# Kernel optimization log

Measured on AMD Instinct MI355X. Metric: run time of the kernel, lower is better.

## Reference

```python
import jax, jax.numpy as jnp
import numpy as np
from jax import lax

B, T, V, E, H, C, K = 256, 512, 50000, 128, 256, 128, 2


def setup_inputs() -> dict:
    key = jax.random.key(0)
    ks = jax.random.split(key, 16)
    s = lambda *sh: 1.0 / np.sqrt(sh[0])
    return {
        "input_current": jax.random.randint(ks[0], (B, T), 0, V, dtype=jnp.int32),
        "input_left": jax.random.randint(ks[1], (B, T), 0, V, dtype=jnp.int32),
        "input_right": jax.random.randint(ks[2], (B, T), 0, V, dtype=jnp.int32),
        "emb": jax.random.normal(ks[3], (V, E), jnp.float32) * 0.05,
        "Wf": jax.random.normal(ks[4], (E, H), jnp.float32) * s(E),
        "Uf": jax.random.normal(ks[5], (H, H), jnp.float32) * s(H),
        "bf": jnp.zeros((H,), jnp.float32),
        "Wb": jax.random.normal(ks[6], (E, H), jnp.float32) * s(E),
        "Ub": jax.random.normal(ks[7], (H, H), jnp.float32) * s(H),
        "bb": jnp.zeros((H,), jnp.float32),
        "Wc": jax.random.normal(ks[8], (2 * H + E, C), jnp.float32) * s(2 * H + E),
        "bc": jnp.zeros((C,), jnp.float32),
        "Wd": jax.random.normal(ks[9], (C, K), jnp.float32) * s(C),
        "bd": jnp.zeros((K,), jnp.float32),
    }


def _simple_rnn(x, W, U, b):
    # x: [B,T,E] -> outputs [B,T,H]; h_t = tanh(x_t W + b + h_{t-1} U)
    xw = jnp.einsum("bte,eh->bth", x, W) + b  # precompute input projection
    h0 = jnp.zeros((x.shape[0], U.shape[0]), x.dtype)

    def step(h, xw_t):
        h = jnp.tanh(xw_t + h @ U)
        return h, h

    _, hs = lax.scan(step, h0, jnp.swapaxes(xw, 0, 1))  # scan over time
    return jnp.swapaxes(hs, 0, 1)


def reference(input_current, input_left, input_right, emb, Wf, Uf, bf, Wb, Ub, bb, Wc, bc, Wd, bd):
    e_cur = emb[input_current]  # [B,T,E]
    e_left = emb[input_left]
    e_right = emb[input_right]
    x_left = _simple_rnn(e_left, Wf, Uf, bf)  # [B,T,H]
    # go_backwards RNN: process reversed sequence, then model reverses back
    x_right = _simple_rnn(e_right[:, ::-1], Wb, Ub, bb)[:, ::-1]  # [B,T,H]
    x = jnp.concatenate([x_left, e_cur, x_right], axis=2)  # [B,T,2H+E]
    x = jnp.tanh(jnp.einsum("btd,dc->btc", x, Wc) + bc)  # Conv1D k=1 + tanh
    x = jnp.max(x, axis=1)  # GlobalMaxPooling1D
    return jax.nn.sigmoid(x @ Wd + bd)  # [B,K]
```

## Files before the change

kernel.cpp:

```cpp
#include <hip/hip_runtime.h>
#include <hip/hip_bf16.h>


#define B_ 256
#define T_ 512
#define E_ 128
#define H_ 256
#define C_ 128

typedef __attribute__((ext_vector_type(8))) short short8;
typedef __attribute__((ext_vector_type(4))) float float4v;
typedef __attribute__((ext_vector_type(2))) unsigned int uint2v;

__device__ inline unsigned short f2bf(float f) {
  unsigned u = __float_as_uint(f);
  u += 0x7fffu + ((u >> 16) & 1u);
  return (unsigned short)(u >> 16);
}
__device__ inline unsigned pkbf(float a, float b) {
  __hip_bfloat162 h2 = __float22bfloat162_rn(float2{a, b});
  union { __hip_bfloat162 h; unsigned u; } cv;
  cv.h = h2;
  return cv.u;
}
__device__ inline float lo16f(unsigned u) { return __uint_as_float(u << 16); }
__device__ inline float hi16f(unsigned u) { return __uint_as_float(u & 0xffff0000u); }
__device__ inline float fast_tanh(float x) {
  float e = __expf(2.f * x);
  float r = __builtin_amdgcn_rcpf(e + 1.f);
  return __builtin_fmaf(-2.f, r, 1.f);
}
__device__ inline unsigned enc_f(float f) {
  unsigned u = __float_as_uint(f);
  return (u & 0x80000000u) ? ~u : (u | 0x80000000u);
}
__device__ inline float dec_f(unsigned key) {
  unsigned bits = (key & 0x80000000u) ? (key ^ 0x80000000u) : ~key;
  return __uint_as_float(bits);
}
__device__ inline void sync_lds() {
  asm volatile("s_waitcnt lgkmcnt(0)\n\ts_barrier" ::: "memory");
}

__device__ inline void st_agent(unsigned short* p, uint2v v) {
  union { uint2v v2; unsigned long long u; } cv;
  cv.v2 = v;
  __hip_atomic_store(reinterpret_cast<unsigned long long*>(p), cv.u,
                     __ATOMIC_RELAXED, __HIP_MEMORY_SCOPE_AGENT);
}

__device__ inline void wait_flag_ge(const int* f, int v) {
  if (__hip_atomic_load(f, __ATOMIC_RELAXED, __HIP_MEMORY_SCOPE_AGENT) < v) {
    while (__hip_atomic_load(f, __ATOMIC_RELAXED, __HIP_MEMORY_SCOPE_AGENT) <
           v)
      __builtin_amdgcn_s_sleep(8);
  }
  (void)__hip_atomic_load(f, __ATOMIC_ACQUIRE, __HIP_MEMORY_SCOPE_AGENT);
}

__global__ __launch_bounds__(256) void prep_kernel(
    const float* __restrict__ Wf, const float* __restrict__ Wb,
    const float* __restrict__ Wc, const float* __restrict__ Uf,
    const float* __restrict__ Ub,
    unsigned short* __restrict__ WfT, unsigned short* __restrict__ WbT,
    unsigned short* __restrict__ WcT, unsigned short* __restrict__ UfT,
    unsigned short* __restrict__ UbT, unsigned int* __restrict__ pooled,
    int* __restrict__ flags) {
  int gid = blockIdx.x * 256 + threadIdx.x;
  int stride = gridDim.x * 256;
  for (int i = gid; i < 128 * 256; i += stride) {
    int k = i >> 8, n = i & 255;
    WfT[n * 128 + k] = f2bf(Wf[i]);
    WbT[n * 128 + k] = f2bf(Wb[i]);
  }
  for (int i = gid; i < 640 * 128; i += stride) {
    int k = i >> 7, n = i & 127;
    WcT[n * 640 + k] = f2bf(Wc[i]);
  }
  for (int i = gid; i < 256 * 256; i += stride) {
    int k = i >> 8, n = i & 255;
    UfT[n * 256 + k] = f2bf(Uf[i]);
    UbT[n * 256 + k] = f2bf(Ub[i]);
  }
  for (int i = gid; i < B_ * C_; i += stride) pooled[i] = 0u;
  for (int i = gid; i < 1024; i += stride) flags[i] = 0;
}

__global__ __launch_bounds__(512, 1) void fused_kernel(
    const int* __restrict__ idxL, const int* __restrict__ idxR,
    const int* __restrict__ idxC, const float* __restrict__ emb,
    const unsigned short* __restrict__ WfT,
    const unsigned short* __restrict__ WbT,
    const float* __restrict__ bfv, const float* __restrict__ bbv,
    const unsigned short* __restrict__ UfT,
    const unsigned short* __restrict__ UbT,
    const unsigned short* __restrict__ WcT, const float* __restrict__ bc,
    unsigned short* x, unsigned int* __restrict__ pooled,
    int* __restrict__ flags) {
  const int blk = blockIdx.x;
  const int tid = threadIdx.x;
  const int lane = tid & 63, q = lane >> 4, l15 = lane & 15;

  __shared__ __attribute__((aligned(16))) unsigned short hbuf[2][16][280];

  if (blk < 32) {
    const int dir = blk & 1;
    const int btile = blk >> 1;
    const int b0 = btile * 16;
    const unsigned short* __restrict__ UT = dir ? UbT : UfT;
    const int xoff = dir ? 384 : 0;
    const int tstep = dir ? -1 : 1;
    const int t0 = dir ? (T_ - 1) : 0;
    const ptrdiff_t dstep = (ptrdiff_t)tstep * 640;
    const int wv8 = tid >> 6;
    int* fl = flags + (dir * 16 + btile) * 32;

    unsigned short* hb0 = &hbuf[0][0][0];
    unsigned short* hb1 = &hbuf[1][0][0];
    for (int i = tid; i < 2 * 16 * 280; i += 512) hb0[i] = 0;

    if (wv8 >= 4) {
      __syncthreads();
#pragma unroll 1
      for (int p = 0; p < 256; ++p) {
        sync_lds();
        sync_lds();
      }
      return;
    }
    const int wv = wv8;

    short8 ufr[4][8];
#pragma unroll
    for (int mt = 0; mt < 4; ++mt)
#pragma unroll
      for (int kt = 0; kt < 8; ++kt)
        ufr[mt][kt] = *(const short8*)(UT + (64 * wv + 16 * mt + l15) * H_ +
                                       kt * 32 + q * 8);

    int lastc = dir ? 31 : 0;
    wait_flag_ge(fl + lastc, 1);

    unsigned short* ptrS[4];
    const unsigned short* ptrL[4];
    uint2v curA[4], curB[4];
#pragma unroll
    for (int mt = 0; mt < 4; ++mt) {
      unsigned short* bt = x + (size_t)(b0 + 4 * wv + mt) * T_ * 640 + xoff +
                           lane * 4 + (ptrdiff_t)t0 * 640;
      curA[mt] = *(const uint2v*)(bt);
      curB[mt] = *(const uint2v*)(bt + dstep);
      ptrS[mt] = bt;
      ptrL[mt] = bt + 2 * dstep;
    }

    const unsigned lrd = l15 * 280;
    const unsigned lwr = l15 * 280 + 64 * wv;

    __syncthreads();

#pragma unroll 1
    for (int p = 0; p < 256; ++p) {
      int c = dir ? ((508 - 2 * p) >> 4) : ((2 * p + 3) >> 4);
      c = c < 0 ? 0 : (c > 31 ? 31 : c);
      if (c != lastc) {
        wait_flag_ge(fl + c, 1);
        lastc = c;
      }
      uint2v ldA[4], ldB[4];
      if (p < 255) {
#pragma unroll
        for (int mt = 0; mt < 4; ++mt) {
          ldA[mt] = *(const uint2v*)(ptrL[mt]);
          ldB[mt] = *(const uint2v*)(ptrL[mt] + dstep);
        }
      } else {
#pragma unroll
        for (int mt = 0; mt < 4; ++mt) {
          ldA[mt] = curA[mt];
          ldB[mt] = curB[mt];
        }
      }
#pragma unroll
      for (int mt = 0; mt < 4; ++mt) ptrL[mt] += 2 * dstep;

      {
        short8 afr[8];
#pragma unroll
        for (int kt = 0; kt < 8; ++kt)
          afr[kt] = *(const short8*)(hb0 + lrd + kt * 32 + q * 8);
        float4v acc[4];
#pragma unroll
        for (int mt = 0; mt < 4; ++mt)
          acc[mt] = (float4v){lo16f(curA[mt].x), hi16f(curA[mt].x),
                              lo16f(curA[mt].y), hi16f(curA[mt].y)};
#pragma unroll
        for (int kt = 0; kt < 8; ++kt)
#pragma unroll
          for (int mt = 0; mt < 4; ++mt)
            acc[mt] = __builtin_amdgcn_mfma_f32_16x16x32_bf16(
                ufr[mt][kt], afr[kt], acc[mt], 0, 0, 0);
#pragma unroll
        for (int mt = 0; mt < 4; ++mt) {
          uint2v hv = {pkbf(fast_tanh(acc[mt][0]), fast_tanh(acc[mt][1])),
                       pkbf(fast_tanh(acc[mt][2]), fast_tanh(acc[mt][3]))};
          *(uint2v*)(hb1 + lwr + 16 * mt + 4 * q) = hv;
          st_agent(ptrS[mt], hv);
        }
      }
      sync_lds();

      {
        short8 afr[8];
#pragma unroll
        for (int kt = 0; kt < 8; ++kt)
          afr[kt] = *(const short8*)(hb1 + lrd + kt * 32 + q * 8);
        float4v acc[4];
#pragma unroll
        for (int mt = 0; mt < 4; ++mt)
          acc[mt] = (float4v){lo16f(curB[mt].x), hi16f(curB[mt].x),
                              lo16f(curB[mt].y), hi16f(curB[mt].y)};
#pragma unroll
        for (int kt = 0; kt < 8; ++kt)
#pragma unroll
          for (int mt = 0; mt < 4; ++mt)
            acc[mt] = __builtin_amdgcn_mfma_f32_16x16x32_bf16(
                ufr[mt][kt], afr[kt], acc[mt], 0, 0, 0);
#pragma unroll
        for (int mt = 0; mt < 4; ++mt) {
          uint2v hv = {pkbf(fast_tanh(acc[mt][0]), fast_tanh(acc[mt][1])),
                       pkbf(fast_tanh(acc[mt][2]), fast_tanh(acc[mt][3]))};
          *(uint2v*)(hb0 + lwr + 16 * mt + 4 * q) = hv;
          st_agent(ptrS[mt] + dstep, hv);
        }
      }
#pragma unroll
      for (int mt = 0; mt < 4; ++mt) {
        ptrS[mt] += 2 * dstep;
        curA[mt] = ldA[mt];
        curB[mt] = ldB[mt];
      }
      if (((p + 1) & 7) == 0) {
        asm volatile("s_waitcnt vmcnt(0) lgkmcnt(0)\n\ts_barrier" ::: "memory");
        if (tid == 0) {
          const int cdone = dir ? (32 - ((p + 1) >> 3)) : (((p + 1) >> 3) - 1);
          __hip_atomic_store(fl + cdone, 2, __ATOMIC_RELAXED,
                             __HIP_MEMORY_SCOPE_AGENT);
        }
      } else {
        sync_lds();
      }
    }
    return;
  }

  if (blk < 1056) {
    const int b2 = blk - 32;
    const int z = b2 >> 5, r = b2 & 31;
    const int btile = r & 15, dirg = r >> 4;
    const int chunk = dirg ? (31 - z) : z;
    const int w8 = tid >> 6;
    const int g = w8 >> 2, wv = w8 & 3;
    const int t0 = chunk * 16 + g * 8;
    const int b0 = btile * 16;
    const int* __restrict__ idx = dirg ? idxR : idxL;
    const unsigned short* __restrict__ WT = dirg ? WbT : WfT;
    const float* __restrict__ bias = dirg ? bbv : bfv;

    short8 wfr[4][4];
#pragma unroll
    for (int mt = 0; mt < 4; ++mt)
#pragma unroll
      for (int kt = 0; kt < 4; ++kt)
        wfr[mt][kt] = *(const short8*)(WT + (64 * wv + 16 * mt + l15) * 128 +
                                       kt * 32 + q * 8);
    float4v bv[4];
#pragma unroll
    for (int mt = 0; mt < 4; ++mt)
      bv[mt] = *(const float4v*)(bias + 64 * wv + 16 * mt + 4 * q);

    int er[8];
#pragma unroll
    for (int j = 0; j < 8; ++j) er[j] = idx[(b0 + l15) * T_ + t0 + j];

    float4v g0[8];
#pragma unroll
    for (int kt = 0; kt < 4; ++kt) {
      const float* p8 = emb + (size_t)er[0] * E_ + kt * 32 + q * 8;
      g0[2 * kt] = *(const float4v*)p8;
      g0[2 * kt + 1] = *(const float4v*)(p8 + 4);
    }

#pragma unroll 1
    for (int j = 0; j < 8; ++j) {
      float4v gn[8];
      if (j < 7) {
#pragma unroll
        for (int kt = 0; kt < 4; ++kt) {
          const float* p8 = emb + (size_t)er[j + 1] * E_ + kt * 32 + q * 8;
          gn[2 * kt] = *(const float4v*)p8;
          gn[2 * kt + 1] = *(const float4v*)(p8 + 4);
        }
      }
      short8 efr[4];
#pragma unroll
      for (int kt = 0; kt < 4; ++kt) {
        union { unsigned u[4]; short8 s; } cv;
        cv.u[0] = pkbf(g0[2 * kt][0], g0[2 * kt][1]);
        cv.u[1] = pkbf(g0[2 * kt][2], g0[2 * kt][3]);
        cv.u[2] = pkbf(g0[2 * kt + 1][0], g0[2 * kt + 1][1]);
        cv.u[3] = pkbf(g0[2 * kt + 1][2], g0[2 * kt + 1][3]);
        efr[kt] = cv.s;
      }
      float4v acc[4];
#pragma unroll
      for (int mt = 0; mt < 4; ++mt) acc[mt] = (float4v){0.f, 0.f, 0.f, 0.f};
#pragma unroll
      for (int kt = 0; kt < 4; ++kt)
#pragma unroll
        for (int mt = 0; mt < 4; ++mt)
          acc[mt] = __builtin_amdgcn_mfma_f32_16x16x32_bf16(
              wfr[mt][kt], efr[kt], acc[mt], 0, 0, 0);
      const int t = t0 + j;
#pragma unroll
      for (int mt = 0; mt < 4; ++mt) {
        float4v v = acc[mt] + bv[mt];
        uint2v pk = {pkbf(v[0], v[1]), pkbf(v[2], v[3])};
        st_agent(x + ((size_t)(b0 + 4 * wv + mt) * T_ + t) * 640 +
                     dirg * 384 + lane * 4,
                 pk);
      }
      if (j < 7) {
#pragma unroll
        for (int kk = 0; kk < 8; ++kk) g0[kk] = gn[kk];
      }
    }
    __syncthreads();
    if (tid == 0) {
      __hip_atomic_store(flags + (dirg * 16 + btile) * 32 + chunk, 1,
                         __ATOMIC_RELAXED, __HIP_MEMORY_SCOPE_AGENT);
    }
    return;
  }

  {
    extern __shared__ unsigned short dtile[];
    const int b2 = blk - 1056;
    const int btile = b2 & 15, g = b2 >> 4;
    const int b0 = btile * 16;
    const int w = tid >> 6;

    short8 wfr[20];
#pragma unroll
    for (int kt = 0; kt < 20; ++kt)
      wfr[kt] =
          *(const short8*)(WcT + (size_t)(16 * w + l15) * 640 + kt * 32 + q * 8);
    float4v bv = *(const float4v*)(bc + 16 * w + 4 * q);

    float4v mx = (float4v){-1e30f, -1e30f, -1e30f, -1e30f};

    const int* flF = flags + btile * 32;
    const int* flB = flags + (16 + btile) * 32;

    const int srow = tid >> 4;
    const int tt0 = srow >> 4, row0 = srow & 15;
    const int ssub = tid & 15;
    const int f0 = 16 * (row0 & 7) + 8 * (row0 >> 3);

#pragma unroll 1
    for (int s = 0; s < 4; ++s) {
      const int rk = g + 8 * s;
      const int c = (rk & 1) ? (16 + (rk >> 1)) : (15 - (rk >> 1));
      wait_flag_ge(flF + c, 2);
      wait_flag_ge(flB + c, 2);
      const int t0c = c * 16;

      auto stage = [&](int jp, int buf) {
        const int t = t0c + 2 * jp + tt0;
        const unsigned short* src = x + ((size_t)(b0 + row0) * T_ + t) * 640;
        unsigned short* dst =
            dtile + (size_t)((buf * 2 + tt0) * 16 + row0) * 648;
        *(short8*)(dst + ssub * 8) = *(const short8*)(src + ssub * 8);
        *(short8*)(dst + 128 + ssub * 8) = *(const short8*)(src + 128 + ssub * 8);
        *(short8*)(dst + 384 + ssub * 8) = *(const short8*)(src + 384 + ssub * 8);
        *(short8*)(dst + 512 + ssub * 8) = *(const short8*)(src + 512 + ssub * 8);
        const int er = idxC[(b0 + ssub) * T_ + t];
        const float* ep = emb + (size_t)er * E_ + f0;
        float4v e0 = *(const float4v*)ep;
        float4v e1 = *(const float4v*)(ep + 4);
        *(uint2v*)(dst + 256 + 4 * ssub) =
            (uint2v){pkbf(e0[0], e0[1]), pkbf(e0[2], e0[3])};
        *(uint2v*)(dst + 320 + 4 * ssub) =
            (uint2v){pkbf(e1[0], e1[1]), pkbf(e1[2], e1[3])};
      };

      stage(0, 0);
      __syncthreads();
#pragma unroll 1
      for (int jp = 0; jp < 8; ++jp) {
        const int buf = jp & 1;
        if (jp < 7) stage(jp + 1, buf ^ 1);
        float4v acc0 = (float4v){0.f, 0.f, 0.f, 0.f};
        float4v acc1 = acc0;
#pragma unroll
        for (int kt = 0; kt < 20; ++kt) {
          int rrow, so1, so2;
          if (kt < 8) {
            rrow = 2 * kt + (q >> 1);
            so1 = 128 * (q & 1) + 4 * l15;
            so2 = so1 + 64;
          } else if (kt < 12) {
            rrow = 2 * (kt - 8) + (q >> 1) + 8 * (q & 1);
            so1 = 256 + 4 * l15;
            so2 = 320 + 4 * l15;
          } else {
            rrow = 2 * (kt - 12) + (q >> 1);
            so1 = 384 + 128 * (q & 1) + 4 * l15;
            so2 = so1 + 64;
          }
          const unsigned short* r0p =
              dtile + (size_t)((buf * 2) * 16 + rrow) * 648;
          const unsigned short* r1p = r0p + 16 * 648;
          uint2v a1 = *(const uint2v*)(r0p + so1);
          uint2v a2 = *(const uint2v*)(r0p + so2);
          uint2v b1 = *(const uint2v*)(r1p + so1);
          uint2v b2 = *(const uint2v*)(r1p + so2);
          union { unsigned u[4]; short8 s8; } cva, cvb;
          cva.u[0] = a1.x; cva.u[1] = a1.y; cva.u[2] = a2.x; cva.u[3] = a2.y;
          cvb.u[0] = b1.x; cvb.u[1] = b1.y; cvb.u[2] = b2.x; cvb.u[3] = b2.y;
          acc0 = __builtin_amdgcn_mfma_f32_16x16x32_bf16(wfr[kt], cva.s8,
                                                         acc0, 0, 0, 0);
          acc1 = __builtin_amdgcn_mfma_f32_16x16x32_bf16(wfr[kt], cvb.s8,
                                                         acc1, 0, 0, 0);
        }
#pragma unroll
        for (int i = 0; i < 4; ++i)
          mx[i] = fmaxf(fmaxf(mx[i], acc0[i]), acc1[i]);
        __syncthreads();
      }
    }
#pragma unroll
    for (int i = 0; i < 4; ++i)
      atomicMax(pooled + (b0 + l15) * C_ + 16 * w + 4 * q + i,
                enc_f(fast_tanh(mx[i] + bv[i])));
  }
}

__global__ __launch_bounds__(256) void dense_kernel(
    const unsigned int* __restrict__ pooled, const float* __restrict__ Wd,
    const float* __restrict__ bd, float* __restrict__ out) {
  int b = threadIdx.x;
  float s0 = bd[0], s1 = bd[1];
#pragma unroll 4
  for (int c = 0; c < C_; ++c) {
    float f = dec_f(pooled[b * C_ + c]);
    s0 += f * Wd[c * 2 + 0];
    s1 += f * Wd[c * 2 + 1];
  }
  out[b * 2 + 0] = 1.f / (1.f + __expf(-s0));
  out[b * 2 + 1] = 1.f / (1.f + __expf(-s1));
}

extern "C" void kernel_launch(void* const* d_in, const int* in_sizes, int n_in,
                              void* d_out, int out_size, void* d_ws, size_t ws_size,
                              hipStream_t stream) {
  const int* idxC = (const int*)d_in[0];
  const int* idxL = (const int*)d_in[1];
  const int* idxR = (const int*)d_in[2];
  const float* emb = (const float*)d_in[3];
  const float* Wf = (const float*)d_in[4];
  const float* Uf = (const float*)d_in[5];
  const float* bf_ = (const float*)d_in[6];
  const float* Wb = (const float*)d_in[7];
  const float* Ub = (const float*)d_in[8];
  const float* bb_ = (const float*)d_in[9];
  const float* Wc = (const float*)d_in[10];
  const float* bc = (const float*)d_in[11];
  const float* Wd = (const float*)d_in[12];
  const float* bd = (const float*)d_in[13];

  char* ws = (char*)d_ws;
  unsigned short* x = (unsigned short*)ws;
  unsigned int* pooled = (unsigned int*)(ws + 167772160);
  unsigned short* WfT = (unsigned short*)(ws + 167903232);
  unsigned short* WbT = WfT + 256 * 128;
  unsigned short* WcT = WbT + 256 * 128;
  unsigned short* UfT = WcT + 128 * 640;
  unsigned short* UbT = UfT + 256 * 256;
  int* flags = (int*)(ws + 168460288);

  prep_kernel<<<64, 256, 0, stream>>>(Wf, Wb, Wc, Uf, Ub, WfT, WbT, WcT, UfT,
                                      UbT, pooled, flags);
  fused_kernel<<<1184, 512, 120 * 1024, stream>>>(idxL, idxR, idxC, emb, WfT,
                                                  WbT, bf_, bb_, UfT, UbT, WcT,
                                                  bc, x, pooled, flags);
  dense_kernel<<<1, 256, 0, stream>>>(pooled, Wd, bd, (float*)d_out);
}
```

Baseline: 665.0 us.

## Prefetch chunk flags, defer done-flag publication, and retune launch attributes

The recurrent blocks now read the next chunk's readiness flag ahead of time, so they only spin when that chunk is not yet ready. They also relax the per-8-step wait from vmcnt(0) to vmcnt(16), publishing each chunk-done flag one period later. The prep kernel now writes the transposed weights coalesced and reads strided, the fused kernel asks for 2 waves per EU, and the dense kernel is split across 4 blocks. Delaying the flag publication adds latency for downstream consumers, and the relaxed waitcnt only stays correct because publication is deferred by one period.

```diff
diff --git a/kernel.cpp b/kernel.cpp
--- a/kernel.cpp
+++ b/kernel.cpp
@@ -68,25 +68,26 @@
     int* __restrict__ flags) {
   int gid = blockIdx.x * 256 + threadIdx.x;
   int stride = gridDim.x * 256;
-  for (int i = gid; i < 128 * 256; i += stride) {
-    int k = i >> 8, n = i & 255;
-    WfT[n * 128 + k] = f2bf(Wf[i]);
-    WbT[n * 128 + k] = f2bf(Wb[i]);
-  }
-  for (int i = gid; i < 640 * 128; i += stride) {
-    int k = i >> 7, n = i & 127;
-    WcT[n * 640 + k] = f2bf(Wc[i]);
+  for (int i = gid; i < 256 * 128; i += stride) {
+    int n = i >> 7, k = i & 127;
+    WfT[i] = f2bf(Wf[k * 256 + n]);
+    WbT[i] = f2bf(Wb[k * 256 + n]);
+  }
+  for (int i = gid; i < 128 * 640; i += stride) {
+    int n = i / 640, k = i - n * 640;
+    WcT[i] = f2bf(Wc[k * 128 + n]);
   }
   for (int i = gid; i < 256 * 256; i += stride) {
-    int k = i >> 8, n = i & 255;
-    UfT[n * 256 + k] = f2bf(Uf[i]);
-    UbT[n * 256 + k] = f2bf(Ub[i]);
+    int n = i >> 8, k = i & 255;
+    UfT[i] = f2bf(Uf[k * 256 + n]);
+    UbT[i] = f2bf(Ub[k * 256 + n]);
   }
   for (int i = gid; i < B_ * C_; i += stride) pooled[i] = 0u;
   for (int i = gid; i < 1024; i += stride) flags[i] = 0;
 }
 
-__global__ __launch_bounds__(512, 1) void fused_kernel(
+__global__ __attribute__((amdgpu_flat_work_group_size(512, 512),
+                          amdgpu_waves_per_eu(2, 2))) void fused_kernel(
     const int* __restrict__ idxL, const int* __restrict__ idxR,
     const int* __restrict__ idxC, const float* __restrict__ emb,
     const unsigned short* __restrict__ WfT,
@@ -117,7 +118,7 @@
 
     unsigned short* hb0 = &hbuf[0][0][0];
     unsigned short* hb1 = &hbuf[1][0][0];
-    for (int i = tid; i < 2 * 16 * 280; i += 512) hb0[i] = 0;
+    for (int i = tid; i < 16 * 280; i += 512) hb0[i] = 0;
 
     if (wv8 >= 4) {
       __syncthreads();
@@ -126,6 +127,7 @@
         sync_lds();
         sync_lds();
       }
+      __syncthreads();
       return;
     }
     const int wv = wv8;
@@ -140,6 +142,9 @@
 
     int lastc = dir ? 31 : 0;
     wait_flag_ge(fl + lastc, 1);
+    int fpre = __hip_atomic_load(fl + (dir ? 30 : 1), __ATOMIC_ACQUIRE,
+                                 __HIP_MEMORY_SCOPE_AGENT);
+    int pending = -1;
 
     unsigned short* ptrS[4];
     const unsigned short* ptrL[4];
@@ -164,8 +169,13 @@
       int c = dir ? ((508 - 2 * p) >> 4) : ((2 * p + 3) >> 4);
       c = c < 0 ? 0 : (c > 31 ? 31 : c);
       if (c != lastc) {
-        wait_flag_ge(fl + c, 1);
+        if (fpre < 1) wait_flag_ge(fl + c, 1);
         lastc = c;
+        const int nc = c + (dir ? -1 : 1);
+        fpre = (nc >= 0 && nc < 32)
+                   ? __hip_atomic_load(fl + nc, __ATOMIC_ACQUIRE,
+                                       __HIP_MEMORY_SCOPE_AGENT)
+                   : 1;
       }
       uint2v ldA[4], ldB[4];
       if (p < 255) {
@@ -241,16 +251,21 @@
         curB[mt] = ldB[mt];
       }
       if (((p + 1) & 7) == 0) {
-        asm volatile("s_waitcnt vmcnt(0) lgkmcnt(0)\n\ts_barrier" ::: "memory");
-        if (tid == 0) {
-          const int cdone = dir ? (32 - ((p + 1) >> 3)) : (((p + 1) >> 3) - 1);
-          __hip_atomic_store(fl + cdone, 2, __ATOMIC_RELAXED,
+        asm volatile("s_waitcnt vmcnt(16) lgkmcnt(0)\n\ts_barrier" :::
+                         "memory");
+        if (tid == 0 && pending >= 0)
+          __hip_atomic_store(fl + pending, 2, __ATOMIC_RELAXED,
                              __HIP_MEMORY_SCOPE_AGENT);
-        }
+        pending = dir ? (32 - ((p + 1) >> 3)) : (((p + 1) >> 3) - 1);
       } else {
         sync_lds();
       }
     }
+    asm volatile("s_waitcnt vmcnt(0)" ::: "memory");
+    __syncthreads();
+    if (tid == 0)
+      __hip_atomic_store(fl + pending, 2, __ATOMIC_RELAXED,
+                         __HIP_MEMORY_SCOPE_AGENT);
     return;
   }
 
@@ -446,10 +461,10 @@
   }
 }
 
-__global__ __launch_bounds__(256) void dense_kernel(
+__global__ __launch_bounds__(64) void dense_kernel(
     const unsigned int* __restrict__ pooled, const float* __restrict__ Wd,
     const float* __restrict__ bd, float* __restrict__ out) {
-  int b = threadIdx.x;
+  int b = blockIdx.x * 64 + threadIdx.x;
   float s0 = bd[0], s1 = bd[1];
 #pragma unroll 4
   for (int c = 0; c < C_; ++c) {
@@ -494,5 +509,5 @@
   fused_kernel<<<1184, 512, 120 * 1024, stream>>>(idxL, idxR, idxC, emb, WfT,
                                                   WbT, bf_, bb_, UfT, UbT, WcT,
                                                   bc, x, pooled, flags);
-  dense_kernel<<<1, 256, 0, stream>>>(pooled, Wd, bd, (float*)d_out);
-}
+  dense_kernel<<<4, 64, 0, stream>>>(pooled, Wd, bd, (float*)d_out);
+}
```

Measured after the change: 647.9 us. 2.6% less time.
